# Performance work log

Measured on AMD Instinct MI355X. Metric: run time of the kernel, lower is better.

The kernel has to match this reference:

```python
import jax, jax.numpy as jnp
import numpy as np
from jax import lax

N_QUBITS = 4
DEPTH = 1
KERNEL = 4
STRIDE = 2


def _ry(theta):
    # RY(theta) = [[cos(t/2), -sin(t/2)], [sin(t/2), cos(t/2)]] (real matrix)
    c, s = jnp.cos(theta / 2), jnp.sin(theta / 2)
    return jnp.stack([jnp.stack([c, -s]), jnp.stack([s, c])])


def _apply_1q(state, U, w):
    # state: [N, 2,2,2,2]; wire w lives on axis 1+w (wire 0 = most significant, PennyLane convention)
    state = jnp.moveaxis(state, 1 + w, -1)
    state = state @ U.T
    return jnp.moveaxis(state, -1, 1 + w)


def _apply_cnot(state, c, t):
    state = jnp.moveaxis(state, (1 + c, 1 + t), (-2, -1))
    state = jnp.stack([state[..., 0, :], state[..., 1, ::-1]], axis=-2)
    return jnp.moveaxis(state, (-2, -1), (1 + c, 1 + t))


def _circuit(psi, weights):
    # psi: [N, 16] normalized real amplitudes; entire circuit (RY + CNOT) is real
    state = psi.reshape(-1, 2, 2, 2, 2)
    for d in range(DEPTH):
        for i in range(N_QUBITS):
            state = _apply_1q(state, _ry(weights[d, i]), i)
        for i in range(N_QUBITS):
            state = _apply_cnot(state, i, (i + 1) % N_QUBITS)
        for i in range(N_QUBITS):
            state = _apply_1q(state, _ry(weights[d, N_QUBITS + i]), i)
    probs = state * state  # real statevector -> |amp|^2
    z = jnp.array([1.0, -1.0], dtype=state.dtype)
    # <Z_w> for each wire
    return jnp.stack([
        jnp.einsum('nabcd,a->n', probs, z),
        jnp.einsum('nabcd,b->n', probs, z),
        jnp.einsum('nabcd,c->n', probs, z),
        jnp.einsum('nabcd,d->n', probs, z)], axis=-1)  # [N, 4]


def setup_inputs() -> dict:
    key = jax.random.key(0)
    k1, k2 = jax.random.split(key)
    x = jax.random.normal(k1, (8192, 1, 32, 32), dtype=jnp.float32)
    weights = jax.random.normal(k2, (DEPTH, 2 * N_QUBITS), dtype=jnp.float32)
    return {"x": x, "weights": weights}


def reference(x, weights):
    B = x.shape[0]
    # zero-pad right/bottom so truncated border slices become zero-padded amplitude inputs
    xp = jnp.pad(x, ((0, 0), (0, 0), (0, STRIDE), (0, STRIDE)))
    # [B, 16, Hp, Wp]; with C=1 features are the row-major flattened 4x4 patch
    patches = lax.conv_general_dilated_patches(
        xp, (KERNEL, KERNEL), (STRIDE, STRIDE), 'VALID')
    Hp, Wp = patches.shape[2], patches.shape[3]
    P = Hp * Wp
    v = patches.reshape(B, KERNEL * KERNEL, P).transpose(0, 2, 1)
    v = v.reshape(B * P, KERNEL * KERNEL)
    # AmplitudeEmbedding(normalize=True)
    psi = v / jnp.linalg.norm(v, axis=-1, keepdims=True)
    exps = _circuit(psi, weights)           # [B*P, 4]
    return exps.reshape(B, P * N_QUBITS)    # patch-major concat, matches torch.cat order
```

## Files before the change

### kernel.cpp

```cpp
#include <hip/hip_runtime.h>
#include <math.h>


#define TS 34

#define RY(M, C, S)                                                    \
    {                                                                  \
        _Pragma("unroll") for (int k = 0; k < 16; ++k) {               \
            if ((k & (M)) == 0) {                                      \
                float a0 = st[k], a1 = st[k | (M)];                    \
                st[k]       = (C) * a0 - (S) * a1;                     \
                st[k | (M)] = (S) * a0 + (C) * a1;                     \
            }                                                          \
        }                                                              \
    }

#define CNOT(MC, MT)                                                   \
    {                                                                  \
        _Pragma("unroll") for (int k = 0; k < 16; ++k) {               \
            if ((k & (MC)) != 0 && (k & (MT)) == 0) {                  \
                float t = st[k];                                       \
                st[k] = st[k | (MT)];                                  \
                st[k | (MT)] = t;                                      \
            }                                                          \
        }                                                              \
    }

#define MEAS(M, CF, SF, OUTV)                                          \
    {                                                                  \
        float A = 0.f, X = 0.f;                                        \
        _Pragma("unroll") for (int k = 0; k < 16; ++k) {               \
            if ((k & (M)) == 0) {                                      \
                A += q[k | (M)];                                       \
                X = fmaf(st[k], st[k | (M)], X);                       \
            }                                                          \
        }                                                              \
        float Zb = T - 2.0f * A;                                       \
        OUTV = ((CF) * Zb - (SF) * (2.0f * X)) * inv;                  \
    }

__global__ __launch_bounds__(256) void quanv_kernel(
    const float* __restrict__ x, const float* __restrict__ w,
    float* __restrict__ out)
{
    __shared__ float tile[34 * TS];
    __shared__ float trig[16];

    const int tid = threadIdx.x;
    const int b = blockIdx.x;

    if (tid < 4) {
        float t = w[tid] * 0.5f;
        trig[tid]     = cosf(t);
        trig[4 + tid] = sinf(t);
    } else if (tid < 8) {
        float t = w[tid];
        trig[4 + tid] = cosf(t);
        trig[8 + tid] = sinf(t);
    }

    const float4 xin = *(const float4*)(x + (size_t)b * 1024 + (tid << 2));
    {
        int row = tid >> 3, col = (tid & 7) << 2;
        float* dst = &tile[row * TS + col];
        *(float2*)(dst)     = make_float2(xin.x, xin.y);
        *(float2*)(dst + 2) = make_float2(xin.z, xin.w);
    }
    if (tid < 68) {
        tile[32 * TS + tid] = 0.f;
    } else if (tid < 132) {
        int k = tid - 68;
        tile[(k >> 1) * TS + 32 + (k & 1)] = 0.f;
    }
    __syncthreads();

    const int py = tid >> 4, px = tid & 15;
    const float* pp = &tile[(py << 1) * TS + (px << 1)];
    float st[16];
#pragma unroll
    for (int dr = 0; dr < 4; ++dr) {
        float2 u0 = *(const float2*)(pp + dr * TS);
        float2 u1 = *(const float2*)(pp + dr * TS + 2);
        st[dr * 4 + 0] = u0.x;
        st[dr * 4 + 1] = u0.y;
        st[dr * 4 + 2] = u1.x;
        st[dr * 4 + 3] = u1.y;
    }

    const float c0 = trig[0], c1 = trig[1], c2 = trig[2], c3 = trig[3];
    const float s0 = trig[4], s1 = trig[5], s2 = trig[6], s3 = trig[7];
    const float cf0 = trig[8],  cf1 = trig[9],  cf2 = trig[10], cf3 = trig[11];
    const float sf0 = trig[12], sf1 = trig[13], sf2 = trig[14], sf3 = trig[15];

    RY(8, c0, s0)
    RY(4, c1, s1)
    RY(2, c2, s2)
    RY(1, c3, s3)

    CNOT(8, 4)
    CNOT(4, 2)
    CNOT(2, 1)
    CNOT(1, 8)

    float q[16];
#pragma unroll
    for (int k = 0; k < 16; ++k) q[k] = st[k] * st[k];
    float T = ((q[0] + q[1]) + (q[2] + q[3])) + ((q[4] + q[5]) + (q[6] + q[7])) +
              (((q[8] + q[9]) + (q[10] + q[11])) + ((q[12] + q[13]) + (q[14] + q[15])));
    float inv = 1.0f / T;

    float e0, e1, e2, e3;
    MEAS(8, cf0, sf0, e0)
    MEAS(4, cf1, sf1, e1)
    MEAS(2, cf2, sf2, e2)
    MEAS(1, cf3, sf3, e3)

    *(float4*)(out + (size_t)b * 1024 + (tid << 2)) = make_float4(e0, e1, e2, e3);
}

extern "C" void kernel_launch(void* const* d_in, const int* in_sizes, int n_in,
                              void* d_out, int out_size, void* d_ws, size_t ws_size,
                              hipStream_t stream) {
    const float* x = (const float*)d_in[0];
    const float* w = (const float*)d_in[1];
    float* out = (float*)d_out;
    const int B = in_sizes[0] >> 10;
    quanv_kernel<<<B, 256, 0, stream>>>(x, w, out);
}
```

Baseline: 89.40 us.

## Read patches directly from global memory and process several images per block

Drops the shared-memory tile and its barrier, so each thread loads its overlapping 4x4 patch straight from global memory and zero-pads the borders with bounds checks. Trig coefficients are computed per lane and broadcast with readlane instead of going through shared memory. Each block now loops over four images, which spreads the trig setup over more work and cuts the grid size. In exchange, overlapping patches cause redundant global loads that rely on the cache, and the loads are less coalesced. The launch also assumes the batch size is divisible by four.

```diff
diff --git a/kernel.cpp b/kernel.cpp
--- a/kernel.cpp
+++ b/kernel.cpp
@@ -2,7 +2,11 @@
 #include <math.h>
 
 
-#define TS 34
+#define IPB 4
+
+__device__ __forceinline__ float rdl(float v, int l) {
+    return __int_as_float(__builtin_amdgcn_readlane(__float_as_int(v), l));
+}
 
 #define RY(M, C, S)                                                    \
     {                                                                  \
@@ -43,79 +47,67 @@
     const float* __restrict__ x, const float* __restrict__ w,
     float* __restrict__ out)
 {
-    __shared__ float tile[34 * TS];
-    __shared__ float trig[16];
+    const int tid  = threadIdx.x;
+    const int lane = tid & 63;
 
-    const int tid = threadIdx.x;
-    const int b = blockIdx.x;
-
-    if (tid < 4) {
-        float t = w[tid] * 0.5f;
-        trig[tid]     = cosf(t);
-        trig[4 + tid] = sinf(t);
-    } else if (tid < 8) {
-        float t = w[tid];
-        trig[4 + tid] = cosf(t);
-        trig[8 + tid] = sinf(t);
-    }
-
-    const float4 xin = *(const float4*)(x + (size_t)b * 1024 + (tid << 2));
-    {
-        int row = tid >> 3, col = (tid & 7) << 2;
-        float* dst = &tile[row * TS + col];
-        *(float2*)(dst)     = make_float2(xin.x, xin.y);
-        *(float2*)(dst + 2) = make_float2(xin.z, xin.w);
-    }
-    if (tid < 68) {
-        tile[32 * TS + tid] = 0.f;
-    } else if (tid < 132) {
-        int k = tid - 68;
-        tile[(k >> 1) * TS + 32 + (k & 1)] = 0.f;
-    }
-    __syncthreads();
+    const float wv  = w[lane & 7];
+    const float ang = ((lane & 7) < 4) ? wv * 0.5f : wv;
+    const float cv = cosf(ang);
+    const float sv = sinf(ang);
+    const float c0 = rdl(cv, 0), c1 = rdl(cv, 1), c2 = rdl(cv, 2), c3 = rdl(cv, 3);
+    const float s0 = rdl(sv, 0), s1 = rdl(sv, 1), s2 = rdl(sv, 2), s3 = rdl(sv, 3);
+    const float cf0 = rdl(cv, 4), cf1 = rdl(cv, 5), cf2 = rdl(cv, 6), cf3 = rdl(cv, 7);
+    const float sf0 = rdl(sv, 4), sf1 = rdl(sv, 5), sf2 = rdl(sv, 6), sf3 = rdl(sv, 7);
 
     const int py = tid >> 4, px = tid & 15;
-    const float* pp = &tile[(py << 1) * TS + (px << 1)];
-    float st[16];
+    const int r0 = py << 1, cc0 = px << 1;
+    const bool cfull = (px < 15);
+    const int rlim = 32 - r0;
+
+    for (int i = 0; i < IPB; ++i) {
+        const size_t b = (size_t)blockIdx.x * IPB + i;
+        const float* __restrict__ pp = x + b * 1024 + r0 * 32 + cc0;
+
+        float st[16];
 #pragma unroll
-    for (int dr = 0; dr < 4; ++dr) {
-        float2 u0 = *(const float2*)(pp + dr * TS);
-        float2 u1 = *(const float2*)(pp + dr * TS + 2);
-        st[dr * 4 + 0] = u0.x;
-        st[dr * 4 + 1] = u0.y;
-        st[dr * 4 + 2] = u1.x;
-        st[dr * 4 + 3] = u1.y;
+        for (int dr = 0; dr < 4; ++dr) {
+            float2 u0 = make_float2(0.f, 0.f);
+            float2 u1 = make_float2(0.f, 0.f);
+            if (dr < rlim) {
+                u0 = *(const float2*)(pp + dr * 32);
+                if (cfull) u1 = *(const float2*)(pp + dr * 32 + 2);
+            }
+            st[dr * 4 + 0] = u0.x;
+            st[dr * 4 + 1] = u0.y;
+            st[dr * 4 + 2] = u1.x;
+            st[dr * 4 + 3] = u1.y;
+        }
+
+        RY(8, c0, s0)
+        RY(4, c1, s1)
+        RY(2, c2, s2)
+        RY(1, c3, s3)
+
+        CNOT(8, 4)
+        CNOT(4, 2)
+        CNOT(2, 1)
+        CNOT(1, 8)
+
+        float q[16];
+#pragma unroll
+        for (int k = 0; k < 16; ++k) q[k] = st[k] * st[k];
+        float T = ((q[0] + q[1]) + (q[2] + q[3])) + ((q[4] + q[5]) + (q[6] + q[7])) +
+                  (((q[8] + q[9]) + (q[10] + q[11])) + ((q[12] + q[13]) + (q[14] + q[15])));
+        float inv = 1.0f / T;
+
+        float e0, e1, e2, e3;
+        MEAS(8, cf0, sf0, e0)
+        MEAS(4, cf1, sf1, e1)
+        MEAS(2, cf2, sf2, e2)
+        MEAS(1, cf3, sf3, e3)
+
+        *(float4*)(out + b * 1024 + (tid << 2)) = make_float4(e0, e1, e2, e3);
     }
-
-    const float c0 = trig[0], c1 = trig[1], c2 = trig[2], c3 = trig[3];
-    const float s0 = trig[4], s1 = trig[5], s2 = trig[6], s3 = trig[7];
-    const float cf0 = trig[8],  cf1 = trig[9],  cf2 = trig[10], cf3 = trig[11];
-    const float sf0 = trig[12], sf1 = trig[13], sf2 = trig[14], sf3 = trig[15];
-
-    RY(8, c0, s0)
-    RY(4, c1, s1)
-    RY(2, c2, s2)
-    RY(1, c3, s3)
-
-    CNOT(8, 4)
-    CNOT(4, 2)
-    CNOT(2, 1)
-    CNOT(1, 8)
-
-    float q[16];
-#pragma unroll
-    for (int k = 0; k < 16; ++k) q[k] = st[k] * st[k];
-    float T = ((q[0] + q[1]) + (q[2] + q[3])) + ((q[4] + q[5]) + (q[6] + q[7])) +
-              (((q[8] + q[9]) + (q[10] + q[11])) + ((q[12] + q[13]) + (q[14] + q[15])));
-    float inv = 1.0f / T;
-
-    float e0, e1, e2, e3;
-    MEAS(8, cf0, sf0, e0)
-    MEAS(4, cf1, sf1, e1)
-    MEAS(2, cf2, sf2, e2)
-    MEAS(1, cf3, sf3, e3)
-
-    *(float4*)(out + (size_t)b * 1024 + (tid << 2)) = make_float4(e0, e1, e2, e3);
 }
 
 extern "C" void kernel_launch(void* const* d_in, const int* in_sizes, int n_in,
@@ -125,5 +117,5 @@
     const float* w = (const float*)d_in[1];
     float* out = (float*)d_out;
     const int B = in_sizes[0] >> 10;
-    quanv_kernel<<<B, 256, 0, stream>>>(x, w, out);
+    quanv_kernel<<<B / IPB, 256, 0, stream>>>(x, w, out);
 }
```

Measured after the change: 90.56 us. Within noise of the previous version (+1.3%).
